# Kernel tuning notes

Measured on AMD Instinct MI355X. Metric: run time of the kernel, lower is better.

## Reference

```python
import jax, jax.numpy as jnp
import numpy as np

N, D_IN, D_OUT, C = 4096, 512, 16384, 256
THRESHOLD = 0.01
TEMPERATURE = 0.1


def setup_inputs() -> dict:
    key = jax.random.key(0)
    k1, k2, k3, k4, k5 = jax.random.split(key, 5)
    inp = jax.random.normal(k1, (N, D_IN), dtype=jnp.float32)
    # kaiming_uniform(a=sqrt(5)) ~ U(-1/sqrt(fan_in), 1/sqrt(fan_in)) scale
    bound = 1.0 / np.sqrt(D_IN)
    weight = jax.random.uniform(k2, (D_OUT, D_IN), minval=-bound, maxval=bound, dtype=jnp.float32)
    bias = jax.random.uniform(k3, (D_OUT,), minval=-bound, maxval=bound, dtype=jnp.float32)
    centroids = jax.random.normal(k4, (C, D_IN), dtype=jnp.float32) * bound
    # disjoint partition of output rows into clusters (stand-in for kmeans labels)
    assignment = jax.random.randint(k5, (D_OUT,), 0, C, dtype=jnp.int32)
    return {"input": inp, "weight": weight, "bias": bias,
            "centroids": centroids, "assignment": assignment}


def reference(input, weight, bias, centroids, assignment):
    # routing: softmax over centroid similarities, threshold
    dots = jax.nn.softmax((input @ centroids.T) / TEMPERATURE, axis=-1)  # [N, C]
    active = dots > THRESHOLD                                            # [N, C] bool
    # torch.unique(query_indices) -> queries active for ANY cluster
    qmask = jnp.any(active, axis=1)                                      # [N]
    # torch.unique(cluster_indices) -> clusters active for ANY query (global union)
    cmask = jnp.any(active, axis=0)                                      # [C]
    # concat(unpad(indices[top_clusters])) -> output rows in any active cluster
    row_mask = cmask[assignment]                                         # [D_OUT]
    # out[top_q].index_copy(1, top_rows, linear(...)); rest stays zero
    dense = input @ weight.T + bias                                      # [N, D_OUT]
    out = dense * qmask[:, None].astype(dense.dtype) * row_mask[None, :].astype(dense.dtype)
    return out
```

## Files before the change

kernel.cpp:

```cpp
#include <hip/hip_runtime.h>
#include <stdint.h>

#define N_Q    4096
#define D_K    512
#define D_OUT  16384
#define NCLUST 256

#define BM 256
#define BN 256
#define BK 32
#define NT (D_K / BK)

typedef __attribute__((ext_vector_type(4))) float f32x4;
typedef __attribute__((ext_vector_type(8))) short bf16x8;

__device__ __forceinline__ uint32_t f2bf(float f) {
  uint32_t u = __float_as_uint(f);
  u += 0x7FFFu + ((u >> 16) & 1u);
  return u >> 16;
}

#define GLOAD_LDS16(g, l)                                         \
  __builtin_amdgcn_global_load_lds(                               \
      (const __attribute__((address_space(1))) void*)(g),         \
      (__attribute__((address_space(3))) void*)(l), 16, 0, 0)

#define WAIT_BAR(N) asm volatile("s_waitcnt vmcnt(" #N ")\n\ts_barrier" ::: "memory")

__global__ __launch_bounds__(256) void cvt_bf16_kernel(const float* __restrict__ src,
                                                       ushort* __restrict__ dst, int n8) {
  int i = blockIdx.x * 256 + threadIdx.x;
  if (i >= n8) return;
  const float4* s = reinterpret_cast<const float4*>(src) + (size_t)i * 2;
  float4 v0 = s[0], v1 = s[1];
  uint4 o;
  o.x = f2bf(v0.x) | (f2bf(v0.y) << 16);
  o.y = f2bf(v0.z) | (f2bf(v0.w) << 16);
  o.z = f2bf(v1.x) | (f2bf(v1.y) << 16);
  o.w = f2bf(v1.z) | (f2bf(v1.w) << 16);
  reinterpret_cast<uint4*>(dst)[i] = o;
}

__global__ __launch_bounds__(256) void transpose_cent_kernel(const float* __restrict__ cent,
                                                             float4* __restrict__ centT4,
                                                             float* __restrict__ cmask) {
  if (blockIdx.x == 0) cmask[threadIdx.x] = 0.0f;
  int idx = blockIdx.x * 256 + threadIdx.x;
  int k4 = idx & 127, c = idx >> 7;
  float4 v = *reinterpret_cast<const float4*>(&cent[(size_t)c * D_K + k4 * 4]);
  centT4[(size_t)k4 * NCLUST + c] = v;
}

__global__ __launch_bounds__(256) void routing_kernel(const float* __restrict__ input,
                                                      const float4* __restrict__ centT4,
                                                      float* __restrict__ qmask,
                                                      float* __restrict__ cmask,
                                                      ushort* __restrict__ A_bf) {
  __shared__ float lgs[8][NCLUST];
  int c = threadIdx.x;
  int q0 = blockIdx.x * 8;
  const float* __restrict__ inp = input + (size_t)q0 * D_K;

  {
    const float4* s4 = reinterpret_cast<const float4*>(inp) + c * 4;
    float4 x0 = s4[0], x1 = s4[1], x2 = s4[2], x3 = s4[3];
    uint4 o0, o1;
    o0.x = f2bf(x0.x) | (f2bf(x0.y) << 16);
    o0.y = f2bf(x0.z) | (f2bf(x0.w) << 16);
    o0.z = f2bf(x1.x) | (f2bf(x1.y) << 16);
    o0.w = f2bf(x1.z) | (f2bf(x1.w) << 16);
    o1.x = f2bf(x2.x) | (f2bf(x2.y) << 16);
    o1.y = f2bf(x2.z) | (f2bf(x2.w) << 16);
    o1.z = f2bf(x3.x) | (f2bf(x3.y) << 16);
    o1.w = f2bf(x3.z) | (f2bf(x3.w) << 16);
    uint4* dst = reinterpret_cast<uint4*>(A_bf + (size_t)q0 * D_K);
    dst[c * 2] = o0;
    dst[c * 2 + 1] = o1;
  }

  float acc[8] = {0, 0, 0, 0, 0, 0, 0, 0};
  for (int k4 = 0; k4 < D_K / 4; ++k4) {
    float4 v = centT4[(size_t)k4 * NCLUST + c];
#pragma unroll
    for (int q = 0; q < 8; ++q) {
      float4 r = *reinterpret_cast<const float4*>(&inp[q * D_K + k4 * 4]);
      acc[q] += v.x * r.x + v.y * r.y + v.z * r.z + v.w * r.w;
    }
  }
#pragma unroll
  for (int q = 0; q < 8; ++q) lgs[q][c] = acc[q] * 10.0f;
  __syncthreads();

  int wave = c >> 6, lane = c & 63;
#pragma unroll
  for (int qq = 0; qq < 2; ++qq) {
    int q = wave * 2 + qq;
    float4 lv = *reinterpret_cast<const float4*>(&lgs[q][lane * 4]);
    float m = fmaxf(fmaxf(lv.x, lv.y), fmaxf(lv.z, lv.w));
#pragma unroll
    for (int off = 32; off > 0; off >>= 1) m = fmaxf(m, __shfl_xor(m, off));
    float e0 = expf(lv.x - m), e1 = expf(lv.y - m), e2 = expf(lv.z - m), e3 = expf(lv.w - m);
    float s = e0 + e1 + e2 + e3;
#pragma unroll
    for (int off = 32; off > 0; off >>= 1) s += __shfl_xor(s, off);
    float thr = 0.01f * s;
    bool a0 = e0 > thr, a1 = e1 > thr, a2 = e2 > thr, a3 = e3 > thr;
    if (a0) cmask[lane * 4 + 0] = 1.0f;
    if (a1) cmask[lane * 4 + 1] = 1.0f;
    if (a2) cmask[lane * 4 + 2] = 1.0f;
    if (a3) cmask[lane * 4 + 3] = 1.0f;
    unsigned long long any = __ballot(a0 | a1 | a2 | a3);
    if (lane == 0) qmask[q0 + q] = any ? 1.0f : 0.0f;
  }
}

__global__ __launch_bounds__(512, 2) void gemm_masked_kernel(
    const ushort* __restrict__ A, const ushort* __restrict__ W,
    const float* __restrict__ bias, const int* __restrict__ assign,
    const float* __restrict__ qmask, const float* __restrict__ cmask,
    float* __restrict__ C) {
  __shared__ ushort sA[3][BM * BK];
  __shared__ ushort sB[3][BN * BK];

  int tid = threadIdx.x;
  int wave = tid >> 6, lane = tid & 63;

  int bid = blockIdx.x;
  int ntile = (bid & 7) * 8 + ((bid >> 3) & 7);
  int mtile = bid >> 6;
  int m0 = mtile * BM, n0 = ntile * BN;

  int wr = wave >> 2, wc = wave & 3;

  const ushort* gA = A + (size_t)m0 * D_K;
  const ushort* gB = W + (size_t)n0 * D_K;

  int srow = tid >> 2;
  int kg = tid & 3;
  int ks = (kg ^ ((srow >> 1) & 3)) * 8;
  const ushort* srcA0 = gA + (size_t)srow * D_K + ks;
  const ushort* srcA1 = gA + (size_t)(128 + srow) * D_K + ks;
  const ushort* srcB0 = gB + (size_t)srow * D_K + ks;
  const ushort* srcB1 = gB + (size_t)(128 + srow) * D_K + ks;
  int ldso = wave * 512;

#define STAGE(buf, kt) do {                              \
    GLOAD_LDS16(srcA0 + (kt), &sA[buf][ldso]);           \
    GLOAD_LDS16(srcA1 + (kt), &sA[buf][4096 + ldso]);    \
    GLOAD_LDS16(srcB0 + (kt), &sB[buf][ldso]);           \
    GLOAD_LDS16(srcB1 + (kt), &sB[buf][4096 + ldso]);    \
  } while (0)

  int kg0 = lane >> 4, l15 = lane & 15;
  int aIdx[8], bIdx[4];
#pragma unroll
  for (int m = 0; m < 8; ++m) {
    int r = wr * 128 + m * 16 + l15;
    aIdx[m] = r * 32 + ((kg0 ^ ((r >> 1) & 3)) << 3);
  }
#pragma unroll
  for (int n = 0; n < 4; ++n) {
    int r = wc * 64 + n * 16 + l15;
    bIdx[n] = r * 32 + ((kg0 ^ ((r >> 1) & 3)) << 3);
  }

  f32x4 acc[8][4] = {};

  STAGE(0, 0);
  STAGE(1, BK);

#pragma unroll
  for (int t = 0; t < NT; ++t) {
    if (t < NT - 1) { WAIT_BAR(4); } else { WAIT_BAR(0); }
    if (t + 2 < NT) STAGE((t + 2) % 3, (t + 2) * BK);

    const ushort* sa = sA[t % 3];
    const ushort* sb = sB[t % 3];
    bf16x8 bf[4], af[4], af2[4];
#pragma unroll
    for (int n = 0; n < 4; ++n) bf[n] = *reinterpret_cast<const bf16x8*>(&sb[bIdx[n]]);
#pragma unroll
    for (int m = 0; m < 4; ++m) af[m] = *reinterpret_cast<const bf16x8*>(&sa[aIdx[m]]);
    __builtin_amdgcn_s_setprio(1);
#pragma unroll
    for (int m = 0; m < 4; ++m)
#pragma unroll
      for (int n = 0; n < 4; ++n)
        acc[m][n] = __builtin_amdgcn_mfma_f32_16x16x32_bf16(af[m], bf[n], acc[m][n], 0, 0, 0);
    __builtin_amdgcn_s_setprio(0);
#pragma unroll
    for (int m = 0; m < 4; ++m) af2[m] = *reinterpret_cast<const bf16x8*>(&sa[aIdx[4 + m]]);
    __builtin_amdgcn_s_setprio(1);
#pragma unroll
    for (int m = 0; m < 4; ++m)
#pragma unroll
      for (int n = 0; n < 4; ++n)
        acc[4 + m][n] = __builtin_amdgcn_mfma_f32_16x16x32_bf16(af2[m], bf[n], acc[4 + m][n], 0, 0, 0);
    __builtin_amdgcn_s_setprio(0);
  }
#undef STAGE

  int lr = lane >> 4;
  float4 qm4[8];
#pragma unroll
  for (int m = 0; m < 8; ++m)
    qm4[m] = *reinterpret_cast<const float4*>(&qmask[m0 + wr * 128 + m * 16 + lr * 4]);
#pragma unroll
  for (int n = 0; n < 4; ++n) {
    int col = n0 + wc * 64 + n * 16 + l15;
    float bj = bias[col];
    float rm = cmask[assign[col]];
#pragma unroll
    for (int m = 0; m < 8; ++m) {
      size_t rbase = (size_t)(m0 + wr * 128 + m * 16 + lr * 4);
      C[(rbase + 0) * D_OUT + col] = (acc[m][n][0] + bj) * qm4[m].x * rm;
      C[(rbase + 1) * D_OUT + col] = (acc[m][n][1] + bj) * qm4[m].y * rm;
      C[(rbase + 2) * D_OUT + col] = (acc[m][n][2] + bj) * qm4[m].z * rm;
      C[(rbase + 3) * D_OUT + col] = (acc[m][n][3] + bj) * qm4[m].w * rm;
    }
  }
}

extern "C" void kernel_launch(void* const* d_in, const int* in_sizes, int n_in,
                              void* d_out, int out_size, void* d_ws, size_t ws_size,
                              hipStream_t stream) {
  const float* input     = (const float*)d_in[0];
  const float* weight    = (const float*)d_in[1];
  const float* bias      = (const float*)d_in[2];
  const float* centroids = (const float*)d_in[3];
  const int*   assign    = (const int*)d_in[4];
  float* out = (float*)d_out;

  char* ws = (char*)d_ws;
  ushort* A_bf   = (ushort*)ws;
  ushort* W_bf   = (ushort*)(ws + 4194304);
  float*  qmask  = (float*)(ws + 20971520);
  float*  cmask  = (float*)(ws + 20987904);
  float4* centT4 = (float4*)(ws + 21000192);

  cvt_bf16_kernel<<<(D_OUT * D_K / 8 + 255) / 256, 256, 0, stream>>>(weight, W_bf, D_OUT * D_K / 8);
  transpose_cent_kernel<<<128, 256, 0, stream>>>(centroids, centT4, cmask);
  routing_kernel<<<N_Q / 8, 256, 0, stream>>>(input, centT4, qmask, cmask, A_bf);
  gemm_masked_kernel<<<(N_Q / BM) * (D_OUT / BN), 512, 0, stream>>>(
      A_bf, W_bf, bias, assign, qmask, cmask, out);
}
```

Before: 164.9 us.

## Halve GEMM M-tile, raise occupancy, remap block order, use nontemporal output stores

```diff
diff --git a/kernel.cpp b/kernel.cpp
--- a/kernel.cpp
+++ b/kernel.cpp
@@ -6,7 +6,7 @@
 #define D_OUT  16384
 #define NCLUST 256
 
-#define BM 256
+#define BM 128
 #define BN 256
 #define BK 32
 #define NT (D_K / BK)
@@ -114,7 +114,7 @@
   }
 }
 
-__global__ __launch_bounds__(512, 2) void gemm_masked_kernel(
+__global__ __launch_bounds__(512, 4) void gemm_masked_kernel(
     const ushort* __restrict__ A, const ushort* __restrict__ W,
     const float* __restrict__ bias, const int* __restrict__ assign,
     const float* __restrict__ qmask, const float* __restrict__ cmask,
@@ -126,8 +126,9 @@
   int wave = tid >> 6, lane = tid & 63;
 
   int bid = blockIdx.x;
-  int ntile = (bid & 7) * 8 + ((bid >> 3) & 7);
-  int mtile = bid >> 6;
+  int r2 = bid >> 3;
+  int ntile = (bid & 7) * 8 + (r2 >> 5);
+  int mtile = r2 & 31;
   int m0 = mtile * BM, n0 = ntile * BN;
 
   int wr = wave >> 2, wc = wave & 3;
@@ -139,23 +140,21 @@
   int kg = tid & 3;
   int ks = (kg ^ ((srow >> 1) & 3)) * 8;
   const ushort* srcA0 = gA + (size_t)srow * D_K + ks;
-  const ushort* srcA1 = gA + (size_t)(128 + srow) * D_K + ks;
   const ushort* srcB0 = gB + (size_t)srow * D_K + ks;
   const ushort* srcB1 = gB + (size_t)(128 + srow) * D_K + ks;
   int ldso = wave * 512;
 
 #define STAGE(buf, kt) do {                              \
     GLOAD_LDS16(srcA0 + (kt), &sA[buf][ldso]);           \
-    GLOAD_LDS16(srcA1 + (kt), &sA[buf][4096 + ldso]);    \
     GLOAD_LDS16(srcB0 + (kt), &sB[buf][ldso]);           \
     GLOAD_LDS16(srcB1 + (kt), &sB[buf][4096 + ldso]);    \
   } while (0)
 
   int kg0 = lane >> 4, l15 = lane & 15;
-  int aIdx[8], bIdx[4];
-#pragma unroll
-  for (int m = 0; m < 8; ++m) {
-    int r = wr * 128 + m * 16 + l15;
+  int aIdx[4], bIdx[4];
+#pragma unroll
+  for (int m = 0; m < 4; ++m) {
+    int r = wr * 64 + m * 16 + l15;
     aIdx[m] = r * 32 + ((kg0 ^ ((r >> 1) & 3)) << 3);
   }
 #pragma unroll
@@ -164,23 +163,24 @@
     bIdx[n] = r * 32 + ((kg0 ^ ((r >> 1) & 3)) << 3);
   }
 
-  f32x4 acc[8][4] = {};
+  f32x4 acc[4][4] = {};
 
   STAGE(0, 0);
   STAGE(1, BK);
 
 #pragma unroll
   for (int t = 0; t < NT; ++t) {
-    if (t < NT - 1) { WAIT_BAR(4); } else { WAIT_BAR(0); }
-    if (t + 2 < NT) STAGE((t + 2) % 3, (t + 2) * BK);
+    if (t < NT - 1) { WAIT_BAR(3); } else { WAIT_BAR(0); }
 
     const ushort* sa = sA[t % 3];
     const ushort* sb = sB[t % 3];
-    bf16x8 bf[4], af[4], af2[4];
+    bf16x8 af[4], bf[4];
 #pragma unroll
     for (int n = 0; n < 4; ++n) bf[n] = *reinterpret_cast<const bf16x8*>(&sb[bIdx[n]]);
 #pragma unroll
     for (int m = 0; m < 4; ++m) af[m] = *reinterpret_cast<const bf16x8*>(&sa[aIdx[m]]);
+    if (t + 2 < NT) STAGE((t + 2) % 3, (t + 2) * BK);
+
     __builtin_amdgcn_s_setprio(1);
 #pragma unroll
     for (int m = 0; m < 4; ++m)
@@ -188,35 +188,28 @@
       for (int n = 0; n < 4; ++n)
         acc[m][n] = __builtin_amdgcn_mfma_f32_16x16x32_bf16(af[m], bf[n], acc[m][n], 0, 0, 0);
     __builtin_amdgcn_s_setprio(0);
-#pragma unroll
-    for (int m = 0; m < 4; ++m) af2[m] = *reinterpret_cast<const bf16x8*>(&sa[aIdx[4 + m]]);
-    __builtin_amdgcn_s_setprio(1);
-#pragma unroll
-    for (int m = 0; m < 4; ++m)
-#pragma unroll
-      for (int n = 0; n < 4; ++n)
-        acc[4 + m][n] = __builtin_amdgcn_mfma_f32_16x16x32_bf16(af2[m], bf[n], acc[4 + m][n], 0, 0, 0);
-    __builtin_amdgcn_s_setprio(0);
   }
 #undef STAGE
 
   int lr = lane >> 4;
-  float4 qm4[8];
-#pragma unroll
-  for (int m = 0; m < 8; ++m)
-    qm4[m] = *reinterpret_cast<const float4*>(&qmask[m0 + wr * 128 + m * 16 + lr * 4]);
+  float bj[4], rm[4];
 #pragma unroll
   for (int n = 0; n < 4; ++n) {
     int col = n0 + wc * 64 + n * 16 + l15;
-    float bj = bias[col];
-    float rm = cmask[assign[col]];
-#pragma unroll
-    for (int m = 0; m < 8; ++m) {
-      size_t rbase = (size_t)(m0 + wr * 128 + m * 16 + lr * 4);
-      C[(rbase + 0) * D_OUT + col] = (acc[m][n][0] + bj) * qm4[m].x * rm;
-      C[(rbase + 1) * D_OUT + col] = (acc[m][n][1] + bj) * qm4[m].y * rm;
-      C[(rbase + 2) * D_OUT + col] = (acc[m][n][2] + bj) * qm4[m].z * rm;
-      C[(rbase + 3) * D_OUT + col] = (acc[m][n][3] + bj) * qm4[m].w * rm;
+    bj[n] = bias[col];
+    rm[n] = cmask[assign[col]];
+  }
+#pragma unroll
+  for (int m = 0; m < 4; ++m) {
+    size_t rbase = (size_t)(m0 + wr * 64 + m * 16 + lr * 4);
+    float4 qm = *reinterpret_cast<const float4*>(&qmask[rbase]);
+#pragma unroll
+    for (int n = 0; n < 4; ++n) {
+      int col = n0 + wc * 64 + n * 16 + l15;
+      __builtin_nontemporal_store((acc[m][n][0] + bj[n]) * qm.x * rm[n], &C[(rbase + 0) * D_OUT + col]);
+      __builtin_nontemporal_store((acc[m][n][1] + bj[n]) * qm.y * rm[n], &C[(rbase + 1) * D_OUT + col]);
+      __builtin_nontemporal_store((acc[m][n][2] + bj[n]) * qm.z * rm[n], &C[(rbase + 2) * D_OUT + col]);
+      __builtin_nontemporal_store((acc[m][n][3] + bj[n]) * qm.w * rm[n], &C[(rbase + 3) * D_OUT + col]);
     }
   }
 }
```

New measurement: 191.8 us. 16.3% more time.
